# Kernel optimization log

Hardware: AMD Instinct MI355X
Metric: run time of the kernel (lower is better)

Reference implementation:

```python
import jax, jax.numpy as jnp
import numpy as np

A_COEF, B_COEF, C_COEF = 1.0, 0.1, 10.0
KL_COEF = 0.005
EPS = 1e-6

B, P1, F, P2 = 32, 778, 1538, 3000
PARAM_DIM, LATENT = 61, 64


def setup_inputs() -> dict:
    key = jax.random.key(0)
    ks = jax.random.split(key, 9)
    return {
        "recon_x": jax.random.normal(ks[0], (B, PARAM_DIM), jnp.float32),
        "x": jax.random.normal(ks[1], (B, PARAM_DIM), jnp.float32),
        "mu": jax.random.normal(ks[2], (B, LATENT), jnp.float32),
        "logvar": jax.random.normal(ks[3], (B, LATENT), jnp.float32),
        "recon_xyz": jax.random.normal(ks[4], (B, P1, 3), jnp.float32),
        "hand_xyz": jax.random.normal(ks[5], (B, P1, 3), jnp.float32),
        "hand_faces": jax.random.randint(ks[6], (B, F, 3), 0, P1, jnp.int64),
        "obj_pts": jax.random.normal(ks[7], (B, P2, 3), jnp.float32),
        "v_weights": jax.random.uniform(ks[8], (P1,), jnp.float32),
    }


def _verts_normals_single(verts, faces):
    # verts: (V,3), faces: (F,3). PyTorch3D-style area-weighted vertex normals.
    v0 = verts[faces[:, 0]]
    v1 = verts[faces[:, 1]]
    v2 = verts[faces[:, 2]]
    fn = jnp.cross(v1 - v0, v2 - v0)  # (F,3) ~ 2*area*face_normal
    n = (jnp.zeros_like(verts)
         .at[faces[:, 0]].add(fn)
         .at[faces[:, 1]].add(fn)
         .at[faces[:, 2]].add(fn))
    norm = jnp.linalg.norm(n, axis=-1, keepdims=True)
    return n / jnp.maximum(norm, EPS)


_verts_normals = jax.vmap(_verts_normals_single)


def _sqdist(xp, yp):
    # (B,P1,P2) pairwise squared distances
    x2 = jnp.sum(xp * xp, axis=-1)[:, :, None]
    y2 = jnp.sum(yp * yp, axis=-1)[:, None, :]
    return x2 + y2 - 2.0 * jnp.einsum('bpd,bqd->bpq', xp, yp)


def _point2point_signed(xp, yp, x_normals):
    # xp: (B,P1,3) hand, yp: (B,P2,3) object, x_normals: (B,P1,3)
    d2 = _sqdist(xp, yp)
    xidx = jnp.argmin(d2, axis=2)  # (B,P1) nearest object point per hand vert
    yidx = jnp.argmin(d2, axis=1)  # (B,P2) nearest hand vert per object point
    x_near = jnp.take_along_axis(yp, xidx[..., None], axis=1)  # (B,P1,3)
    y_near = jnp.take_along_axis(xp, yidx[..., None], axis=1)  # (B,P2,3)
    x2y = xp - x_near
    y2x = yp - y_near
    y_nn = jnp.take_along_axis(x_normals, yidx[..., None], axis=1)  # (B,P2,3)
    in_out = jnp.sign(jnp.sum(y_nn * y2x, axis=-1))
    y2x_signed = jnp.linalg.norm(y2x, axis=2) * in_out  # (B,P2)
    x2y_signed = jnp.linalg.norm(x2y, axis=2)           # (B,P1)
    return y2x_signed, x2y_signed


def _loss_cnet(verts_rhand, verts_rhand_gt, faces, verts_obj, v_weights):
    v_w2 = jnp.power(v_weights, 1.0 / 2.5)
    rh_n = _verts_normals(verts_rhand, faces)
    rh_n_gt = _verts_normals(verts_rhand_gt, faces)
    o2h, h2o = _point2point_signed(verts_rhand, verts_obj, rh_n)
    o2h_gt, h2o_gt = _point2point_signed(verts_rhand_gt, verts_obj, rh_n_gt)
    w_dist = (o2h_gt < 0.01) & (o2h_gt > -0.005)
    w_neg = o2h < 0.0
    w = jnp.where(w_neg, 1.5, jnp.where(w_dist, 1.0, 0.1))
    loss_h = 35.0 * (1.0 - KL_COEF) * jnp.mean(jnp.abs(jnp.abs(h2o) - jnp.abs(h2o_gt)) * v_w2)
    loss_o = 30.0 * (1.0 - KL_COEF) * jnp.mean(jnp.abs(o2h - o2h_gt) * w)
    return loss_h + loss_o


def reference(recon_x, x, mu, logvar, recon_xyz, hand_xyz, hand_faces, obj_pts, v_weights):
    bsz = recon_x.shape[0]
    param_loss = jnp.sum((recon_x - x) ** 2) / bsz
    recon_loss = jnp.sum((recon_xyz - hand_xyz) ** 2) / hand_xyz.shape[0]
    KLD = -0.5 * jnp.sum(1.0 + logvar - mu ** 2 - jnp.exp(logvar)) / hand_xyz.shape[0]
    cvae_loss = recon_loss + KLD
    ho_loss = _loss_cnet(recon_xyz, hand_xyz, hand_faces, obj_pts, v_weights)
    loss = A_COEF * cvae_loss + B_COEF * param_loss + C_COEF * ho_loss
    return loss, param_loss, ho_loss, recon_loss, KLD
```

## Files before the change

### kernel.cpp

```cpp
#include <hip/hip_runtime.h>
#include <math.h>

#define B 32
#define P1 778
#define NF 1538
#define P2 3000
#define PARAM_DIM 61
#define LATENT 64

#define P1PAD 784
#define NTH 49
#define CHO 192
#define NTO 12
#define NTOH 6
#define NCH 16
#define NPART NCH

#define RED1_BLKS 16
#define HC_BLKS 128
#define OC_BLKS 192
#define QF 385

#define D1_NRM 256
#define D1_TOT (D1_NRM + RED1_BLKS)
#define D2_TOT (NCH * 64)
#define D3_TOT (OC_BLKS + HC_BLKS)

#define NP_OFF  0
#define NP_SZ   (4*2*B*P1*4)
#define OS_OFF  (NP_OFF + NP_SZ)
#define OS_SZ   (2*B*P2)
#define HP_OFF  (OS_OFF + OS_SZ)
#define HP_SZ   (NPART*2*B*P1PAD)
#define R1_OFF  (HP_OFF + HP_SZ)
#define RH_OFF  (R1_OFF + RED1_BLKS*3)
#define RO_OFF  (RH_OFF + HC_BLKS)

typedef __attribute__((ext_vector_type(8))) short bf16x8;
typedef __attribute__((ext_vector_type(4))) float f32x4;
union U4 { uint4 u; bf16x8 v; };

static __device__ __forceinline__ unsigned umin2(unsigned a, unsigned b) { return a < b ? a : b; }
static __device__ __forceinline__ unsigned bhi(float x) { return __float_as_uint(x) >> 16; }
static __device__ __forceinline__ float bres(float x, unsigned h) { return x - __uint_as_float(h << 16); }

template <int CTRL>
static __device__ __forceinline__ float dpp_min(float x) {
  const int xi = __float_as_int(x);
  const int yi = __builtin_amdgcn_update_dpp(xi, xi, CTRL, 0xF, 0xF, false);
  return fminf(x, __int_as_float(yi));
}
static __device__ __forceinline__ float row_min16(float x) {
  x = dpp_min<0xB1>(x);
  x = dpp_min<0x4E>(x);
  x = dpp_min<0x124>(x);
  x = dpp_min<0x128>(x);
  return x;
}

__global__ __launch_bounds__(256) void kd1(
    const float* __restrict__ recon_x, const float* __restrict__ x,
    const float* __restrict__ mu, const float* __restrict__ logvar,
    const float* __restrict__ recon_xyz, const float* __restrict__ hand_xyz,
    const int* __restrict__ faces, float* __restrict__ ws) {
  __shared__ float4 sv[P1];
  __shared__ float sn[4][2336];
  const int tid = threadIdx.x;
  const int bid = blockIdx.x;

  if (bid < D1_NRM) {
    const int q = bid >> 6, r = bid & 63, set = r >> 5, b = r & 31;
    const float* verts = (set == 0 ? recon_xyz : hand_xyz) + b * P1 * 3;
    const int* f = faces + b * NF * 3 + q * QF * 3;
    const int nf = (q < 3) ? QF : (NF - 3 * QF);
    for (int i = tid; i < P1; i += 256)
      sv[i] = make_float4(verts[3*i], verts[3*i+1], verts[3*i+2], 0.f);
    for (int i = tid; i < 4 * 2336; i += 256) ((float*)sn)[i] = 0.f;
    __syncthreads();
    float* s = sn[tid >> 6];
    for (int k = tid; k < nf; k += 256) {
      int i0 = f[3*k], i1 = f[3*k+1], i2 = f[3*k+2];
      float4 v0 = sv[i0], v1 = sv[i1], v2 = sv[i2];
      float e0x = v1.x - v0.x, e0y = v1.y - v0.y, e0z = v1.z - v0.z;
      float e1x = v2.x - v0.x, e1y = v2.y - v0.y, e1z = v2.z - v0.z;
      float fx = e0y * e1z - e0z * e1y;
      float fy = e0z * e1x - e0x * e1z;
      float fz = e0x * e1y - e0y * e1x;
      atomicAdd(&s[3*i0+0], fx); atomicAdd(&s[3*i0+1], fy); atomicAdd(&s[3*i0+2], fz);
      atomicAdd(&s[3*i1+0], fx); atomicAdd(&s[3*i1+1], fy); atomicAdd(&s[3*i1+2], fz);
      atomicAdd(&s[3*i2+0], fx); atomicAdd(&s[3*i2+1], fy); atomicAdd(&s[3*i2+2], fz);
    }
    __syncthreads();
    float4* np = (float4*)(ws + NP_OFF) + (size_t)((q * 2 + set) * B + b) * P1;
    for (int p = tid; p < P1; p += 256) {
      float nx = sn[0][3*p] + sn[1][3*p] + sn[2][3*p] + sn[3][3*p];
      float ny = sn[0][3*p+1] + sn[1][3*p+1] + sn[2][3*p+1] + sn[3][3*p+1];
      float nz = sn[0][3*p+2] + sn[1][3*p+2] + sn[2][3*p+2] + sn[3][3*p+2];
      np[p] = make_float4(nx, ny, nz, 0.f);
    }
  } else {
    const int blk = bid - D1_NRM;
    const int gtid = blk * 256 + tid, stride = RED1_BLKS * 256;
    float sp = 0.f, sr = 0.f, sk = 0.f;
    for (int i = gtid; i < B * PARAM_DIM; i += stride) { float d = recon_x[i] - x[i]; sp += d * d; }
    for (int i = gtid; i < B * P1 * 3; i += stride)    { float d = recon_xyz[i] - hand_xyz[i]; sr += d * d; }
    for (int i = gtid; i < B * LATENT; i += stride)    { float lv = logvar[i], m = mu[i]; sk += 1.f + lv - m * m - expf(lv); }
    for (int off = 32; off > 0; off >>= 1) {
      sp += __shfl_down(sp, off, 64);
      sr += __shfl_down(sr, off, 64);
      sk += __shfl_down(sk, off, 64);
    }
    float* sred = (float*)sn;
    const int wv = tid >> 6;
    if ((tid & 63) == 0) { sred[wv*3] = sp; sred[wv*3+1] = sr; sred[wv*3+2] = sk; }
    __syncthreads();
    if (tid == 0) {
      float a = 0.f, bb = 0.f, c = 0.f;
      for (int w = 0; w < 4; ++w) { a += sred[w*3]; bb += sred[w*3+1]; c += sred[w*3+2]; }
      ws[R1_OFF + blk*3+0] = a; ws[R1_OFF + blk*3+1] = bb; ws[R1_OFF + blk*3+2] = c;
    }
  }
}

__global__ __launch_bounds__(256, 4) void kd2(
    const float* __restrict__ recon_xyz, const float* __restrict__ hand_xyz,
    const float* __restrict__ obj, float* __restrict__ ws) {
  __shared__ float4 sVerts[P1PAD];
  __shared__ float4 sObj[CHO];
  __shared__ unsigned sKeys[4][CHO];

  const int tid = threadIdx.x;
  const int bid = blockIdx.x;
  const int chunk = bid >> 6, rr = bid & 63, set = rr >> 5, b = rr & 31;
  const float* verts = (set == 0 ? recon_xyz : hand_xyz) + b * P1 * 3;
  const float* op = obj + (size_t)b * P2 * 3;

  for (int i = tid; i < P1PAD; i += 256) {
    float vx, vy, vz;
    if (i < P1) { vx = verts[3*i]; vy = verts[3*i+1]; vz = verts[3*i+2]; }
    else        { vx = vy = vz = 1.0e6f; }
    sVerts[i] = make_float4(vx, vy, vz, vx*vx + vy*vy + vz*vz);
  }
  for (int i = tid; i < CHO; i += 256) {
    const int q = chunk * CHO + i;
    float ox, oy, oz;
    if (q < P2) { ox = op[3*q]; oy = op[3*q+1]; oz = op[3*q+2]; }
    else        { ox = oy = oz = 1.0e6f; }
    sObj[i] = make_float4(ox, oy, oz, ox*ox + oy*oy + oz*oz);
  }
  __syncthreads();

  const int l = tid & 63, wv = tid >> 6, g = l >> 4, cl = l & 15;
  U4 bw[NTO];
  #pragma unroll
  for (int j = 0; j < NTO; ++j) {
    const float4 o = sObj[j * 16 + cl];
    unsigned u0 = 0u, u1 = 0u, u2 = 0u, u3 = 0u;
    if (g == 0) {
      const unsigned ohx = bhi(o.x), ohy = bhi(o.y), ohz = bhi(o.z);
      const unsigned olx = bhi(bres(o.x, ohx));
      const unsigned oly = bhi(bres(o.y, ohy));
      u0 = ohx | (ohy << 16);
      u1 = ohz | (ohx << 16);
      u2 = ohy | (ohz << 16);
      u3 = olx | (oly << 16);
    } else if (g == 1) {
      const unsigned ohz = bhi(o.z);
      const unsigned olz = bhi(bres(o.z, ohz));
      const float o2p = o.w + 1.0f;
      const unsigned o2h = bhi(o2p);
      const unsigned o2l = bhi(bres(o2p, o2h));
      u0 = olz | (0x3F80u << 16);
      u1 = 0x3F80u | (o2h << 16);
      u2 = o2l;
      u3 = 0u;
    }
    bw[j].u = make_uint4(u0, u1, u2, u3);
  }

  unsigned om[NTO];
  #pragma unroll
  for (int j = 0; j < NTO; ++j) om[j] = 0xFFFFFFFFu;

  float* hpart = ws + HP_OFF + (size_t)(((chunk * 2) + set) * B + b) * P1PAD;
  const f32x4 czero = {0.f, 0.f, 0.f, 0.f};
  const int nt = (NTH - wv + 3) >> 2;

  for (int s = 0; s < nt; ++s) {
    const int t = wv + 4 * s;
    const int ib = t * 16 + g * 4;
    U4 ac;
    if (l < 32) {
      const float4 v = sVerts[t * 16 + cl];
      if (g == 0) {
        const float sx = -2.f * v.x, sy = -2.f * v.y, sz = -2.f * v.z;
        const unsigned hx = bhi(sx), hy = bhi(sy), hz = bhi(sz);
        const unsigned lx = bhi(bres(sx, hx));
        const unsigned ly = bhi(bres(sy, hy));
        const unsigned lz = bhi(bres(sz, hz));
        ac.u = make_uint4(hx | (hy << 16), hz | (lx << 16),
                          ly | (lz << 16), hx | (hy << 16));
      } else {
        const float sz = -2.f * v.z;
        const unsigned hz = bhi(sz);
        const unsigned h2h = bhi(v.w);
        const unsigned h2l = bhi(bres(v.w, h2h));
        ac.u = make_uint4(hz | (h2h << 16), h2l | (0x3F80u << 16), 0x3F80u, 0u);
      }
    } else {
      ac.u = make_uint4(0u, 0u, 0u, 0u);
    }
    float hm0 = 3.0e38f, hm1 = 3.0e38f, hm2 = 3.0e38f, hm3 = 3.0e38f;
    #pragma unroll
    for (int hs = 0; hs < 2; ++hs) {
      f32x4 dd[NTOH];
      #pragma unroll
      for (int j = 0; j < NTOH; ++j)
        dd[j] = __builtin_amdgcn_mfma_f32_16x16x32_bf16(ac.v, bw[hs * NTOH + j].v, czero, 0, 0, 0);
      #pragma unroll
      for (int j = 0; j < NTOH; ++j) {
        const f32x4 d = dd[j];
        hm0 = fminf(hm0, d[0]); hm1 = fminf(hm1, d[1]);
        hm2 = fminf(hm2, d[2]); hm3 = fminf(hm3, d[3]);
        const unsigned k0 = (__float_as_uint(d[0]) & 0xFFFFFC00u) | (unsigned)(ib + 0);
        const unsigned k1 = (__float_as_uint(d[1]) & 0xFFFFFC00u) | (unsigned)(ib + 1);
        const unsigned k2 = (__float_as_uint(d[2]) & 0xFFFFFC00u) | (unsigned)(ib + 2);
        const unsigned k3 = (__float_as_uint(d[3]) & 0xFFFFFC00u) | (unsigned)(ib + 3);
        om[hs * NTOH + j] = umin2(umin2(umin2(umin2(k0, k1), k2), k3), om[hs * NTOH + j]);
      }
    }
    hm0 = row_min16(hm0);
    hm1 = row_min16(hm1);
    hm2 = row_min16(hm2);
    hm3 = row_min16(hm3);
    if (cl == 0)
      *(float4*)&hpart[ib] = make_float4(hm0 - 1.f, hm1 - 1.f, hm2 - 1.f, hm3 - 1.f);
  }

  #pragma unroll
  for (int j = 0; j < NTO; ++j) {
    unsigned v = umin2(om[j], (unsigned)__shfl_xor((int)om[j], 16, 64));
    v = umin2(v, (unsigned)__shfl_xor((int)v, 32, 64));
    if (l < 16) sKeys[wv][j * 16 + l] = v;
  }
  __syncthreads();

  const float4* npb = (const float4*)(ws + NP_OFF);
  float* os = ws + OS_OFF + (size_t)(set * B + b) * P2;
  for (int i = tid; i < CHO; i += 256) {
    const int q = chunk * CHO + i;
    if (q < P2) {
      const unsigned key = umin2(umin2(sKeys[0][i], sKeys[1][i]),
                                 umin2(sKeys[2][i], sKeys[3][i]));
      int hi = (int)(key & 1023u); if (hi > P1 - 1) hi = P1 - 1;
      const float4 h = sVerts[hi];
      const float4 o = sObj[i];
      const float dx = o.x - h.x, dy = o.y - h.y, dz = o.z - h.z;
      const float d2 = fmaf(dx, dx, fmaf(dy, dy, dz * dz));
      const float4 n0 = npb[(size_t)((0 * 2 + set) * B + b) * P1 + hi];
      const float4 n1 = npb[(size_t)((1 * 2 + set) * B + b) * P1 + hi];
      const float4 n2 = npb[(size_t)((2 * 2 + set) * B + b) * P1 + hi];
      const float4 n3 = npb[(size_t)((3 * 2 + set) * B + b) * P1 + hi];
      const float nx = (n0.x + n1.x) + (n2.x + n3.x);
      const float ny = (n0.y + n1.y) + (n2.y + n3.y);
      const float nz = (n0.z + n1.z) + (n2.z + n3.z);
      const float dt = nx * dx + ny * dy + nz * dz;
      const float sg = (dt > 0.f) ? 1.f : ((dt < 0.f) ? -1.f : 0.f);
      os[q] = sqrtf(d2) * sg;
    }
  }
}

__global__ __launch_bounds__(256) void kd3(const float* __restrict__ vw,
                                           float* __restrict__ ws) {
  __shared__ float sred[4];
  const int tid = threadIdx.x;
  const int bid = blockIdx.x;
  if (bid < OC_BLKS) {
    const int gtid = bid * 256 + tid, stride = OC_BLKS * 256;
    float so = 0.f;
    for (int i = gtid; i < B * P2; i += stride) {
      float osA = ws[OS_OFF + i];
      float osB = ws[OS_OFF + (size_t)B * P2 + i];
      bool wdist = (osB < 0.01f) && (osB > -0.005f);
      float w = (osA < 0.f) ? 1.5f : (wdist ? 1.f : 0.1f);
      so += fabsf(osA - osB) * w;
    }
    for (int off = 32; off > 0; off >>= 1) so += __shfl_down(so, off, 64);
    if ((tid & 63) == 0) sred[tid >> 6] = so;
    __syncthreads();
    if (tid == 0) ws[RO_OFF + bid] = sred[0] + sred[1] + sred[2] + sred[3];
  } else {
    const int blk = bid - OC_BLKS;
    const int gtid = blk * 256 + tid, stride = HC_BLKS * 256;
    float sh = 0.f;
    for (int i = gtid; i < B * P1; i += stride) {
      const int p = i % P1, bb = i / P1;
      const size_t base0 = (size_t)HP_OFF + (size_t)bb * P1PAD + p;
      float m0 = 3.0e38f, m1 = 3.0e38f;
      #pragma unroll
      for (int c = 0; c < NPART; ++c) {
        m0 = fminf(m0, ws[base0 + (size_t)(c*2+0) * B * P1PAD]);
        m1 = fminf(m1, ws[base0 + (size_t)(c*2+1) * B * P1PAD]);
      }
      m0 = fmaxf(m0, 0.f); m1 = fmaxf(m1, 0.f);
      sh += fabsf(sqrtf(m0) - sqrtf(m1)) * powf(vw[p], 0.4f);
    }
    for (int off = 32; off > 0; off >>= 1) sh += __shfl_down(sh, off, 64);
    if ((tid & 63) == 0) sred[tid >> 6] = sh;
    __syncthreads();
    if (tid == 0) ws[RH_OFF + blk] = sred[0] + sred[1] + sred[2] + sred[3];
  }
}

__global__ void kfin(const float* __restrict__ ws, float* __restrict__ out) {
  const int lane = threadIdx.x;
  float sp = 0.f, sr = 0.f, sk = 0.f, sh = 0.f, so = 0.f;
  for (int i = lane; i < RED1_BLKS; i += 64) {
    sp += ws[R1_OFF + i*3+0]; sr += ws[R1_OFF + i*3+1]; sk += ws[R1_OFF + i*3+2];
  }
  for (int i = lane; i < HC_BLKS; i += 64) sh += ws[RH_OFF + i];
  for (int i = lane; i < OC_BLKS; i += 64) so += ws[RO_OFF + i];
  for (int off = 32; off > 0; off >>= 1) {
    sp += __shfl_down(sp, off, 64);
    sr += __shfl_down(sr, off, 64);
    sk += __shfl_down(sk, off, 64);
    sh += __shfl_down(sh, off, 64);
    so += __shfl_down(so, off, 64);
  }
  if (lane == 0) {
    float param_loss = sp / (float)B;
    float recon_loss = sr / (float)B;
    float KLD = -0.5f * sk / (float)B;
    float cvae = recon_loss + KLD;
    float loss_h = 35.f * (1.f - 0.005f) * sh / (float)(B * P1);
    float loss_o = 30.f * (1.f - 0.005f) * so / (float)(B * P2);
    float ho = loss_h + loss_o;
    out[0] = cvae + 0.1f * param_loss + 10.f * ho;
    out[1] = param_loss;
    out[2] = ho;
    out[3] = recon_loss;
    out[4] = KLD;
  }
}

extern "C" void kernel_launch(void* const* d_in, const int* in_sizes, int n_in,
                              void* d_out, int out_size, void* d_ws, size_t ws_size,
                              hipStream_t stream) {
  const float* recon_x   = (const float*)d_in[0];
  const float* x         = (const float*)d_in[1];
  const float* mu        = (const float*)d_in[2];
  const float* logvar    = (const float*)d_in[3];
  const float* recon_xyz = (const float*)d_in[4];
  const float* hand_xyz  = (const float*)d_in[5];
  const int*   faces     = (const int*)d_in[6];
  const float* obj       = (const float*)d_in[7];
  const float* vw        = (const float*)d_in[8];
  float* ws = (float*)d_ws;
  float* out = (float*)d_out;

  kd1<<<dim3(D1_TOT), 256, 0, stream>>>(recon_x, x, mu, logvar,
                                        recon_xyz, hand_xyz, faces, ws);
  kd2<<<dim3(D2_TOT), 256, 0, stream>>>(recon_xyz, hand_xyz, obj, ws);
  kd3<<<dim3(D3_TOT), 256, 0, stream>>>(vw, ws);
  kfin<<<1, 64, 0, stream>>>(ws, out);
}
```

Before: 115.5 us.

## Partition vertex normals by vertex range and fold final reduction into kd3

The normal computation now splits work by vertex range (200 vertices per block) instead of by face range. Each block scans all faces and only accumulates into its own vertices, so a single normal buffer is written and kd2 loads one float4 per lookup instead of four partials. The separate kfin launch is removed: kd3 uses an atomic counter with threadfences so the last block does the final reduction. The cost is redundant face processing in kd1, in exchange for one fewer kernel launch and fewer global reads in kd2.

New measurement: 138.2 us. 1.2x slower.

```diff
diff --git a/kernel.cpp b/kernel.cpp
--- a/kernel.cpp
+++ b/kernel.cpp
@@ -19,7 +19,7 @@
 #define RED1_BLKS 16
 #define HC_BLKS 128
 #define OC_BLKS 192
-#define QF 385
+#define VR 200
 
 #define D1_NRM 256
 #define D1_TOT (D1_NRM + RED1_BLKS)
@@ -27,7 +27,7 @@
 #define D3_TOT (OC_BLKS + HC_BLKS)
 
 #define NP_OFF  0
-#define NP_SZ   (4*2*B*P1*4)
+#define NP_SZ   (2*B*P1*4)
 #define OS_OFF  (NP_OFF + NP_SZ)
 #define OS_SZ   (2*B*P2)
 #define HP_OFF  (OS_OFF + OS_SZ)
@@ -35,6 +35,7 @@
 #define R1_OFF  (HP_OFF + HP_SZ)
 #define RH_OFF  (R1_OFF + RED1_BLKS*3)
 #define RO_OFF  (RH_OFF + HC_BLKS)
+#define CNT_OFF (RO_OFF + OC_BLKS)
 
 typedef __attribute__((ext_vector_type(8))) short bf16x8;
 typedef __attribute__((ext_vector_type(4))) float f32x4;
@@ -64,21 +65,22 @@
     const float* __restrict__ recon_xyz, const float* __restrict__ hand_xyz,
     const int* __restrict__ faces, float* __restrict__ ws) {
   __shared__ float4 sv[P1];
-  __shared__ float sn[4][2336];
+  __shared__ float sn[4][3 * VR];
   const int tid = threadIdx.x;
   const int bid = blockIdx.x;
 
   if (bid < D1_NRM) {
     const int q = bid >> 6, r = bid & 63, set = r >> 5, b = r & 31;
+    const int lo = q * VR;
+    const int hi = (lo + VR < P1) ? lo + VR : P1;
     const float* verts = (set == 0 ? recon_xyz : hand_xyz) + b * P1 * 3;
-    const int* f = faces + b * NF * 3 + q * QF * 3;
-    const int nf = (q < 3) ? QF : (NF - 3 * QF);
+    const int* f = faces + b * NF * 3;
     for (int i = tid; i < P1; i += 256)
       sv[i] = make_float4(verts[3*i], verts[3*i+1], verts[3*i+2], 0.f);
-    for (int i = tid; i < 4 * 2336; i += 256) ((float*)sn)[i] = 0.f;
+    for (int i = tid; i < 4 * 3 * VR; i += 256) ((float*)sn)[i] = 0.f;
     __syncthreads();
     float* s = sn[tid >> 6];
-    for (int k = tid; k < nf; k += 256) {
+    for (int k = tid; k < NF; k += 256) {
       int i0 = f[3*k], i1 = f[3*k+1], i2 = f[3*k+2];
       float4 v0 = sv[i0], v1 = sv[i1], v2 = sv[i2];
       float e0x = v1.x - v0.x, e0y = v1.y - v0.y, e0z = v1.z - v0.z;
@@ -86,20 +88,31 @@
       float fx = e0y * e1z - e0z * e1y;
       float fy = e0z * e1x - e0x * e1z;
       float fz = e0x * e1y - e0y * e1x;
-      atomicAdd(&s[3*i0+0], fx); atomicAdd(&s[3*i0+1], fy); atomicAdd(&s[3*i0+2], fz);
-      atomicAdd(&s[3*i1+0], fx); atomicAdd(&s[3*i1+1], fy); atomicAdd(&s[3*i1+2], fz);
-      atomicAdd(&s[3*i2+0], fx); atomicAdd(&s[3*i2+1], fy); atomicAdd(&s[3*i2+2], fz);
-    }
-    __syncthreads();
-    float4* np = (float4*)(ws + NP_OFF) + (size_t)((q * 2 + set) * B + b) * P1;
-    for (int p = tid; p < P1; p += 256) {
-      float nx = sn[0][3*p] + sn[1][3*p] + sn[2][3*p] + sn[3][3*p];
-      float ny = sn[0][3*p+1] + sn[1][3*p+1] + sn[2][3*p+1] + sn[3][3*p+1];
-      float nz = sn[0][3*p+2] + sn[1][3*p+2] + sn[2][3*p+2] + sn[3][3*p+2];
+      if (i0 >= lo && i0 < hi) {
+        int j = (i0 - lo) * 3;
+        atomicAdd(&s[j+0], fx); atomicAdd(&s[j+1], fy); atomicAdd(&s[j+2], fz);
+      }
+      if (i1 >= lo && i1 < hi) {
+        int j = (i1 - lo) * 3;
+        atomicAdd(&s[j+0], fx); atomicAdd(&s[j+1], fy); atomicAdd(&s[j+2], fz);
+      }
+      if (i2 >= lo && i2 < hi) {
+        int j = (i2 - lo) * 3;
+        atomicAdd(&s[j+0], fx); atomicAdd(&s[j+1], fy); atomicAdd(&s[j+2], fz);
+      }
+    }
+    __syncthreads();
+    float4* np = (float4*)(ws + NP_OFF) + (size_t)(set * B + b) * P1;
+    for (int p = lo + tid; p < hi; p += 256) {
+      const int j = (p - lo) * 3;
+      float nx = sn[0][j]   + sn[1][j]   + sn[2][j]   + sn[3][j];
+      float ny = sn[0][j+1] + sn[1][j+1] + sn[2][j+1] + sn[3][j+1];
+      float nz = sn[0][j+2] + sn[1][j+2] + sn[2][j+2] + sn[3][j+2];
       np[p] = make_float4(nx, ny, nz, 0.f);
     }
   } else {
     const int blk = bid - D1_NRM;
+    if (blk == 0 && tid == 0) ws[CNT_OFF] = 0.f;
     const int gtid = blk * 256 + tid, stride = RED1_BLKS * 256;
     float sp = 0.f, sr = 0.f, sk = 0.f;
     for (int i = gtid; i < B * PARAM_DIM; i += stride) { float d = recon_x[i] - x[i]; sp += d * d; }
@@ -245,7 +258,7 @@
   }
   __syncthreads();
 
-  const float4* npb = (const float4*)(ws + NP_OFF);
+  const float4* np = (const float4*)(ws + NP_OFF) + (size_t)(set * B + b) * P1;
   float* os = ws + OS_OFF + (size_t)(set * B + b) * P2;
   for (int i = tid; i < CHO; i += 256) {
     const int q = chunk * CHO + i;
@@ -257,14 +270,8 @@
       const float4 o = sObj[i];
       const float dx = o.x - h.x, dy = o.y - h.y, dz = o.z - h.z;
       const float d2 = fmaf(dx, dx, fmaf(dy, dy, dz * dz));
-      const float4 n0 = npb[(size_t)((0 * 2 + set) * B + b) * P1 + hi];
-      const float4 n1 = npb[(size_t)((1 * 2 + set) * B + b) * P1 + hi];
-      const float4 n2 = npb[(size_t)((2 * 2 + set) * B + b) * P1 + hi];
-      const float4 n3 = npb[(size_t)((3 * 2 + set) * B + b) * P1 + hi];
-      const float nx = (n0.x + n1.x) + (n2.x + n3.x);
-      const float ny = (n0.y + n1.y) + (n2.y + n3.y);
-      const float nz = (n0.z + n1.z) + (n2.z + n3.z);
-      const float dt = nx * dx + ny * dy + nz * dz;
+      const float4 n = np[hi];
+      const float dt = n.x * dx + n.y * dy + n.z * dz;
       const float sg = (dt > 0.f) ? 1.f : ((dt < 0.f) ? -1.f : 0.f);
       os[q] = sqrtf(d2) * sg;
     }
@@ -272,8 +279,10 @@
 }
 
 __global__ __launch_bounds__(256) void kd3(const float* __restrict__ vw,
-                                           float* __restrict__ ws) {
+                                           float* __restrict__ ws,
+                                           float* __restrict__ out) {
   __shared__ float sred[4];
+  __shared__ int lastFlag;
   const int tid = threadIdx.x;
   const int bid = blockIdx.x;
   if (bid < OC_BLKS) {
@@ -311,36 +320,45 @@
     __syncthreads();
     if (tid == 0) ws[RH_OFF + blk] = sred[0] + sred[1] + sred[2] + sred[3];
   }
-}
-
-__global__ void kfin(const float* __restrict__ ws, float* __restrict__ out) {
-  const int lane = threadIdx.x;
-  float sp = 0.f, sr = 0.f, sk = 0.f, sh = 0.f, so = 0.f;
-  for (int i = lane; i < RED1_BLKS; i += 64) {
-    sp += ws[R1_OFF + i*3+0]; sr += ws[R1_OFF + i*3+1]; sk += ws[R1_OFF + i*3+2];
-  }
-  for (int i = lane; i < HC_BLKS; i += 64) sh += ws[RH_OFF + i];
-  for (int i = lane; i < OC_BLKS; i += 64) so += ws[RO_OFF + i];
-  for (int off = 32; off > 0; off >>= 1) {
-    sp += __shfl_down(sp, off, 64);
-    sr += __shfl_down(sr, off, 64);
-    sk += __shfl_down(sk, off, 64);
-    sh += __shfl_down(sh, off, 64);
-    so += __shfl_down(so, off, 64);
-  }
-  if (lane == 0) {
-    float param_loss = sp / (float)B;
-    float recon_loss = sr / (float)B;
-    float KLD = -0.5f * sk / (float)B;
-    float cvae = recon_loss + KLD;
-    float loss_h = 35.f * (1.f - 0.005f) * sh / (float)(B * P1);
-    float loss_o = 30.f * (1.f - 0.005f) * so / (float)(B * P2);
-    float ho = loss_h + loss_o;
-    out[0] = cvae + 0.1f * param_loss + 10.f * ho;
-    out[1] = param_loss;
-    out[2] = ho;
-    out[3] = recon_loss;
-    out[4] = KLD;
+
+  __threadfence();
+  if (tid == 0) {
+    const int t = atomicAdd((int*)(ws + CNT_OFF), 1);
+    lastFlag = (t == D3_TOT - 1);
+  }
+  __syncthreads();
+  if (lastFlag) {
+    __threadfence();
+    if (tid < 64) {
+      const int lane = tid;
+      float sp = 0.f, sr = 0.f, sk = 0.f, sh = 0.f, so = 0.f;
+      for (int i = lane; i < RED1_BLKS; i += 64) {
+        sp += ws[R1_OFF + i*3+0]; sr += ws[R1_OFF + i*3+1]; sk += ws[R1_OFF + i*3+2];
+      }
+      for (int i = lane; i < HC_BLKS; i += 64) sh += ws[RH_OFF + i];
+      for (int i = lane; i < OC_BLKS; i += 64) so += ws[RO_OFF + i];
+      for (int off = 32; off > 0; off >>= 1) {
+        sp += __shfl_down(sp, off, 64);
+        sr += __shfl_down(sr, off, 64);
+        sk += __shfl_down(sk, off, 64);
+        sh += __shfl_down(sh, off, 64);
+        so += __shfl_down(so, off, 64);
+      }
+      if (lane == 0) {
+        float param_loss = sp / (float)B;
+        float recon_loss = sr / (float)B;
+        float KLD = -0.5f * sk / (float)B;
+        float cvae = recon_loss + KLD;
+        float loss_h = 35.f * (1.f - 0.005f) * sh / (float)(B * P1);
+        float loss_o = 30.f * (1.f - 0.005f) * so / (float)(B * P2);
+        float ho = loss_h + loss_o;
+        out[0] = cvae + 0.1f * param_loss + 10.f * ho;
+        out[1] = param_loss;
+        out[2] = ho;
+        out[3] = recon_loss;
+        out[4] = KLD;
+      }
+    }
   }
 }
 
@@ -362,6 +380,5 @@
   kd1<<<dim3(D1_TOT), 256, 0, stream>>>(recon_x, x, mu, logvar,
                                         recon_xyz, hand_xyz, faces, ws);
   kd2<<<dim3(D2_TOT), 256, 0, stream>>>(recon_xyz, hand_xyz, obj, ws);
-  kd3<<<dim3(D3_TOT), 256, 0, stream>>>(vw, ws);
-  kfin<<<1, 64, 0, stream>>>(ws, out);
-}
+  kd3<<<dim3(D3_TOT), 256, 0, stream>>>(vw, ws, out);
+}
```

## Merge normals and nearest-neighbour kernels, move signing to reduce, fold final sum

Applied to the files above, without the earlier changes.

Fuses the vertex-normal, small-reduction and distance/argmin kernels into one launch with a shared-memory union. This is possible because the signed-distance step that needs the normals now runs in the reduction kernel, which reads the stored argmin keys and recomputes distances and signs. The separate final kernel is replaced by a last-block-done atomic counter, cutting the launch chain from four kernels to two. In exchange the reduce kernel does scattered gathers of vertices and normals, and the normal accumulation uses two shared copies instead of four, so more threads contend on each shared atomic.

Measured after the change: 146.9 us. 27.1% more time.

```diff
diff --git a/kernel.cpp b/kernel.cpp
--- a/kernel.cpp
+++ b/kernel.cpp
@@ -21,9 +21,9 @@
 #define OC_BLKS 192
 #define QF 385
 
-#define D1_NRM 256
-#define D1_TOT (D1_NRM + RED1_BLKS)
-#define D2_TOT (NCH * 64)
+#define M_D2  (NCH * 64)
+#define M_NRM 256
+#define M_TOT (M_D2 + M_NRM + RED1_BLKS)
 #define D3_TOT (OC_BLKS + HC_BLKS)
 
 #define NP_OFF  0
@@ -35,6 +35,7 @@
 #define R1_OFF  (HP_OFF + HP_SZ)
 #define RH_OFF  (R1_OFF + RED1_BLKS*3)
 #define RO_OFF  (RH_OFF + HC_BLKS)
+#define CNT_OFF (RO_OFF + OC_BLKS)
 
 typedef __attribute__((ext_vector_type(8))) short bf16x8;
 typedef __attribute__((ext_vector_type(4))) float f32x4;
@@ -58,29 +59,158 @@
   return x;
 }
 
-__global__ __launch_bounds__(256) void kd1(
+union SMem {
+  struct { float4 sv[P1]; float sn[2][2336]; } d1;
+  struct { float4 sVerts[P1PAD]; float4 sObj[CHO]; unsigned sKeys[4][CHO]; } d2;
+};
+
+__global__ __launch_bounds__(256, 4) void kd12(
     const float* __restrict__ recon_x, const float* __restrict__ x,
     const float* __restrict__ mu, const float* __restrict__ logvar,
     const float* __restrict__ recon_xyz, const float* __restrict__ hand_xyz,
-    const int* __restrict__ faces, float* __restrict__ ws) {
-  __shared__ float4 sv[P1];
-  __shared__ float sn[4][2336];
+    const int* __restrict__ faces, const float* __restrict__ obj,
+    float* __restrict__ ws) {
+  __shared__ SMem sm;
   const int tid = threadIdx.x;
   const int bid = blockIdx.x;
 
-  if (bid < D1_NRM) {
-    const int q = bid >> 6, r = bid & 63, set = r >> 5, b = r & 31;
+  if (bid < M_D2) {
+    const int chunk = bid >> 6, rr = bid & 63, set = rr >> 5, b = rr & 31;
+    const float* verts = (set == 0 ? recon_xyz : hand_xyz) + b * P1 * 3;
+    const float* op = obj + (size_t)b * P2 * 3;
+
+    for (int i = tid; i < P1PAD; i += 256) {
+      float vx, vy, vz;
+      if (i < P1) { vx = verts[3*i]; vy = verts[3*i+1]; vz = verts[3*i+2]; }
+      else        { vx = vy = vz = 1.0e6f; }
+      sm.d2.sVerts[i] = make_float4(vx, vy, vz, vx*vx + vy*vy + vz*vz);
+    }
+    for (int i = tid; i < CHO; i += 256) {
+      const int q = chunk * CHO + i;
+      float ox, oy, oz;
+      if (q < P2) { ox = op[3*q]; oy = op[3*q+1]; oz = op[3*q+2]; }
+      else        { ox = oy = oz = 1.0e6f; }
+      sm.d2.sObj[i] = make_float4(ox, oy, oz, ox*ox + oy*oy + oz*oz);
+    }
+    __syncthreads();
+
+    const int l = tid & 63, wv = tid >> 6, g = l >> 4, cl = l & 15;
+    U4 bw[NTO];
+    #pragma unroll
+    for (int j = 0; j < NTO; ++j) {
+      const float4 o = sm.d2.sObj[j * 16 + cl];
+      unsigned u0 = 0u, u1 = 0u, u2 = 0u, u3 = 0u;
+      if (g == 0) {
+        const unsigned ohx = bhi(o.x), ohy = bhi(o.y), ohz = bhi(o.z);
+        const unsigned olx = bhi(bres(o.x, ohx));
+        const unsigned oly = bhi(bres(o.y, ohy));
+        u0 = ohx | (ohy << 16);
+        u1 = ohz | (ohx << 16);
+        u2 = ohy | (ohz << 16);
+        u3 = olx | (oly << 16);
+      } else if (g == 1) {
+        const unsigned ohz = bhi(o.z);
+        const unsigned olz = bhi(bres(o.z, ohz));
+        const float o2p = o.w + 1.0f;
+        const unsigned o2h = bhi(o2p);
+        const unsigned o2l = bhi(bres(o2p, o2h));
+        u0 = olz | (0x3F80u << 16);
+        u1 = 0x3F80u | (o2h << 16);
+        u2 = o2l;
+        u3 = 0u;
+      }
+      bw[j].u = make_uint4(u0, u1, u2, u3);
+    }
+
+    unsigned om[NTO];
+    #pragma unroll
+    for (int j = 0; j < NTO; ++j) om[j] = 0xFFFFFFFFu;
+
+    float* hpart = ws + HP_OFF + (size_t)(((chunk * 2) + set) * B + b) * P1PAD;
+    const f32x4 czero = {0.f, 0.f, 0.f, 0.f};
+    const int nt = (NTH - wv + 3) >> 2;
+
+    for (int s = 0; s < nt; ++s) {
+      const int t = wv + 4 * s;
+      const int ib = t * 16 + g * 4;
+      U4 ac;
+      if (l < 32) {
+        const float4 v = sm.d2.sVerts[t * 16 + cl];
+        if (g == 0) {
+          const float sx = -2.f * v.x, sy = -2.f * v.y, sz = -2.f * v.z;
+          const unsigned hx = bhi(sx), hy = bhi(sy), hz = bhi(sz);
+          const unsigned lx = bhi(bres(sx, hx));
+          const unsigned ly = bhi(bres(sy, hy));
+          const unsigned lz = bhi(bres(sz, hz));
+          ac.u = make_uint4(hx | (hy << 16), hz | (lx << 16),
+                            ly | (lz << 16), hx | (hy << 16));
+        } else {
+          const float sz = -2.f * v.z;
+          const unsigned hz = bhi(sz);
+          const unsigned h2h = bhi(v.w);
+          const unsigned h2l = bhi(bres(v.w, h2h));
+          ac.u = make_uint4(hz | (h2h << 16), h2l | (0x3F80u << 16), 0x3F80u, 0u);
+        }
+      } else {
+        ac.u = make_uint4(0u, 0u, 0u, 0u);
+      }
+      float hm0 = 3.0e38f, hm1 = 3.0e38f, hm2 = 3.0e38f, hm3 = 3.0e38f;
+      #pragma unroll
+      for (int hs = 0; hs < 2; ++hs) {
+        f32x4 dd[NTOH];
+        #pragma unroll
+        for (int j = 0; j < NTOH; ++j)
+          dd[j] = __builtin_amdgcn_mfma_f32_16x16x32_bf16(ac.v, bw[hs * NTOH + j].v, czero, 0, 0, 0);
+        #pragma unroll
+        for (int j = 0; j < NTOH; ++j) {
+          const f32x4 d = dd[j];
+          hm0 = fminf(hm0, d[0]); hm1 = fminf(hm1, d[1]);
+          hm2 = fminf(hm2, d[2]); hm3 = fminf(hm3, d[3]);
+          const unsigned k0 = (__float_as_uint(d[0]) & 0xFFFFFC00u) | (unsigned)(ib + 0);
+          const unsigned k1 = (__float_as_uint(d[1]) & 0xFFFFFC00u) | (unsigned)(ib + 1);
+          const unsigned k2 = (__float_as_uint(d[2]) & 0xFFFFFC00u) | (unsigned)(ib + 2);
+          const unsigned k3 = (__float_as_uint(d[3]) & 0xFFFFFC00u) | (unsigned)(ib + 3);
+          om[hs * NTOH + j] = umin2(umin2(umin2(umin2(k0, k1), k2), k3), om[hs * NTOH + j]);
+        }
+      }
+      hm0 = row_min16(hm0);
+      hm1 = row_min16(hm1);
+      hm2 = row_min16(hm2);
+      hm3 = row_min16(hm3);
+      if (cl == 0)
+        *(float4*)&hpart[ib] = make_float4(hm0 - 1.f, hm1 - 1.f, hm2 - 1.f, hm3 - 1.f);
+    }
+
+    #pragma unroll
+    for (int j = 0; j < NTO; ++j) {
+      unsigned v = umin2(om[j], (unsigned)__shfl_xor((int)om[j], 16, 64));
+      v = umin2(v, (unsigned)__shfl_xor((int)v, 32, 64));
+      if (l < 16) sm.d2.sKeys[wv][j * 16 + l] = v;
+    }
+    __syncthreads();
+
+    unsigned* os = (unsigned*)(ws + OS_OFF) + (size_t)(set * B + b) * P2;
+    for (int i = tid; i < CHO; i += 256) {
+      const int q = chunk * CHO + i;
+      if (q < P2)
+        os[q] = umin2(umin2(sm.d2.sKeys[0][i], sm.d2.sKeys[1][i]),
+                      umin2(sm.d2.sKeys[2][i], sm.d2.sKeys[3][i]));
+    }
+
+  } else if (bid < M_D2 + M_NRM) {
+    const int t = bid - M_D2;
+    const int q = t >> 6, r = t & 63, set = r >> 5, b = r & 31;
     const float* verts = (set == 0 ? recon_xyz : hand_xyz) + b * P1 * 3;
     const int* f = faces + b * NF * 3 + q * QF * 3;
     const int nf = (q < 3) ? QF : (NF - 3 * QF);
     for (int i = tid; i < P1; i += 256)
-      sv[i] = make_float4(verts[3*i], verts[3*i+1], verts[3*i+2], 0.f);
-    for (int i = tid; i < 4 * 2336; i += 256) ((float*)sn)[i] = 0.f;
-    __syncthreads();
-    float* s = sn[tid >> 6];
+      sm.d1.sv[i] = make_float4(verts[3*i], verts[3*i+1], verts[3*i+2], 0.f);
+    for (int i = tid; i < 2 * 2336; i += 256) ((float*)sm.d1.sn)[i] = 0.f;
+    __syncthreads();
+    float* s = sm.d1.sn[tid >> 7];
     for (int k = tid; k < nf; k += 256) {
       int i0 = f[3*k], i1 = f[3*k+1], i2 = f[3*k+2];
-      float4 v0 = sv[i0], v1 = sv[i1], v2 = sv[i2];
+      float4 v0 = sm.d1.sv[i0], v1 = sm.d1.sv[i1], v2 = sm.d1.sv[i2];
       float e0x = v1.x - v0.x, e0y = v1.y - v0.y, e0z = v1.z - v0.z;
       float e1x = v2.x - v0.x, e1y = v2.y - v0.y, e1z = v2.z - v0.z;
       float fx = e0y * e1z - e0z * e1y;
@@ -93,13 +223,14 @@
     __syncthreads();
     float4* np = (float4*)(ws + NP_OFF) + (size_t)((q * 2 + set) * B + b) * P1;
     for (int p = tid; p < P1; p += 256) {
-      float nx = sn[0][3*p] + sn[1][3*p] + sn[2][3*p] + sn[3][3*p];
-      float ny = sn[0][3*p+1] + sn[1][3*p+1] + sn[2][3*p+1] + sn[3][3*p+1];
-      float nz = sn[0][3*p+2] + sn[1][3*p+2] + sn[2][3*p+2] + sn[3][3*p+2];
+      float nx = sm.d1.sn[0][3*p]   + sm.d1.sn[1][3*p];
+      float ny = sm.d1.sn[0][3*p+1] + sm.d1.sn[1][3*p+1];
+      float nz = sm.d1.sn[0][3*p+2] + sm.d1.sn[1][3*p+2];
       np[p] = make_float4(nx, ny, nz, 0.f);
     }
   } else {
-    const int blk = bid - D1_NRM;
+    const int blk = bid - M_D2 - M_NRM;
+    if (blk == 0 && tid == 0) ((int*)(ws + CNT_OFF))[0] = 0;
     const int gtid = blk * 256 + tid, stride = RED1_BLKS * 256;
     float sp = 0.f, sr = 0.f, sk = 0.f;
     for (int i = gtid; i < B * PARAM_DIM; i += stride) { float d = recon_x[i] - x[i]; sp += d * d; }
@@ -110,7 +241,7 @@
       sr += __shfl_down(sr, off, 64);
       sk += __shfl_down(sk, off, 64);
     }
-    float* sred = (float*)sn;
+    float* sred = (float*)sm.d1.sn;
     const int wv = tid >> 6;
     if ((tid & 63) == 0) { sred[wv*3] = sp; sred[wv*3+1] = sr; sred[wv*3+2] = sk; }
     __syncthreads();
@@ -122,166 +253,46 @@
   }
 }
 
-__global__ __launch_bounds__(256, 4) void kd2(
+__global__ __launch_bounds__(256) void kd3(
+    const float* __restrict__ vw,
     const float* __restrict__ recon_xyz, const float* __restrict__ hand_xyz,
-    const float* __restrict__ obj, float* __restrict__ ws) {
-  __shared__ float4 sVerts[P1PAD];
-  __shared__ float4 sObj[CHO];
-  __shared__ unsigned sKeys[4][CHO];
-
-  const int tid = threadIdx.x;
-  const int bid = blockIdx.x;
-  const int chunk = bid >> 6, rr = bid & 63, set = rr >> 5, b = rr & 31;
-  const float* verts = (set == 0 ? recon_xyz : hand_xyz) + b * P1 * 3;
-  const float* op = obj + (size_t)b * P2 * 3;
-
-  for (int i = tid; i < P1PAD; i += 256) {
-    float vx, vy, vz;
-    if (i < P1) { vx = verts[3*i]; vy = verts[3*i+1]; vz = verts[3*i+2]; }
-    else        { vx = vy = vz = 1.0e6f; }
-    sVerts[i] = make_float4(vx, vy, vz, vx*vx + vy*vy + vz*vz);
-  }
-  for (int i = tid; i < CHO; i += 256) {
-    const int q = chunk * CHO + i;
-    float ox, oy, oz;
-    if (q < P2) { ox = op[3*q]; oy = op[3*q+1]; oz = op[3*q+2]; }
-    else        { ox = oy = oz = 1.0e6f; }
-    sObj[i] = make_float4(ox, oy, oz, ox*ox + oy*oy + oz*oz);
-  }
-  __syncthreads();
-
-  const int l = tid & 63, wv = tid >> 6, g = l >> 4, cl = l & 15;
-  U4 bw[NTO];
-  #pragma unroll
-  for (int j = 0; j < NTO; ++j) {
-    const float4 o = sObj[j * 16 + cl];
-    unsigned u0 = 0u, u1 = 0u, u2 = 0u, u3 = 0u;
-    if (g == 0) {
-      const unsigned ohx = bhi(o.x), ohy = bhi(o.y), ohz = bhi(o.z);
-      const unsigned olx = bhi(bres(o.x, ohx));
-      const unsigned oly = bhi(bres(o.y, ohy));
-      u0 = ohx | (ohy << 16);
-      u1 = ohz | (ohx << 16);
-      u2 = ohy | (ohz << 16);
-      u3 = olx | (oly << 16);
-    } else if (g == 1) {
-      const unsigned ohz = bhi(o.z);
-      const unsigned olz = bhi(bres(o.z, ohz));
-      const float o2p = o.w + 1.0f;
-      const unsigned o2h = bhi(o2p);
-      const unsigned o2l = bhi(bres(o2p, o2h));
-      u0 = olz | (0x3F80u << 16);
-      u1 = 0x3F80u | (o2h << 16);
-      u2 = o2l;
-      u3 = 0u;
-    }
-    bw[j].u = make_uint4(u0, u1, u2, u3);
-  }
-
-  unsigned om[NTO];
-  #pragma unroll
-  for (int j = 0; j < NTO; ++j) om[j] = 0xFFFFFFFFu;
-
-  float* hpart = ws + HP_OFF + (size_t)(((chunk * 2) + set) * B + b) * P1PAD;
-  const f32x4 czero = {0.f, 0.f, 0.f, 0.f};
-  const int nt = (NTH - wv + 3) >> 2;
-
-  for (int s = 0; s < nt; ++s) {
-    const int t = wv + 4 * s;
-    const int ib = t * 16 + g * 4;
-    U4 ac;
-    if (l < 32) {
-      const float4 v = sVerts[t * 16 + cl];
-      if (g == 0) {
-        const float sx = -2.f * v.x, sy = -2.f * v.y, sz = -2.f * v.z;
-        const unsigned hx = bhi(sx), hy = bhi(sy), hz = bhi(sz);
-        const unsigned lx = bhi(bres(sx, hx));
-        const unsigned ly = bhi(bres(sy, hy));
-        const unsigned lz = bhi(bres(sz, hz));
-        ac.u = make_uint4(hx | (hy << 16), hz | (lx << 16),
-                          ly | (lz << 16), hx | (hy << 16));
-      } else {
-        const float sz = -2.f * v.z;
-        const unsigned hz = bhi(sz);
-        const unsigned h2h = bhi(v.w);
-        const unsigned h2l = bhi(bres(v.w, h2h));
-        ac.u = make_uint4(hz | (h2h << 16), h2l | (0x3F80u << 16), 0x3F80u, 0u);
-      }
-    } else {
-      ac.u = make_uint4(0u, 0u, 0u, 0u);
-    }
-    float hm0 = 3.0e38f, hm1 = 3.0e38f, hm2 = 3.0e38f, hm3 = 3.0e38f;
-    #pragma unroll
-    for (int hs = 0; hs < 2; ++hs) {
-      f32x4 dd[NTOH];
-      #pragma unroll
-      for (int j = 0; j < NTOH; ++j)
-        dd[j] = __builtin_amdgcn_mfma_f32_16x16x32_bf16(ac.v, bw[hs * NTOH + j].v, czero, 0, 0, 0);
-      #pragma unroll
-      for (int j = 0; j < NTOH; ++j) {
-        const f32x4 d = dd[j];
-        hm0 = fminf(hm0, d[0]); hm1 = fminf(hm1, d[1]);
-        hm2 = fminf(hm2, d[2]); hm3 = fminf(hm3, d[3]);
-        const unsigned k0 = (__float_as_uint(d[0]) & 0xFFFFFC00u) | (unsigned)(ib + 0);
-        const unsigned k1 = (__float_as_uint(d[1]) & 0xFFFFFC00u) | (unsigned)(ib + 1);
-        const unsigned k2 = (__float_as_uint(d[2]) & 0xFFFFFC00u) | (unsigned)(ib + 2);
-        const unsigned k3 = (__float_as_uint(d[3]) & 0xFFFFFC00u) | (unsigned)(ib + 3);
-        om[hs * NTOH + j] = umin2(umin2(umin2(umin2(k0, k1), k2), k3), om[hs * NTOH + j]);
-      }
-    }
-    hm0 = row_min16(hm0);
-    hm1 = row_min16(hm1);
-    hm2 = row_min16(hm2);
-    hm3 = row_min16(hm3);
-    if (cl == 0)
-      *(float4*)&hpart[ib] = make_float4(hm0 - 1.f, hm1 - 1.f, hm2 - 1.f, hm3 - 1.f);
-  }
-
-  #pragma unroll
-  for (int j = 0; j < NTO; ++j) {
-    unsigned v = umin2(om[j], (unsigned)__shfl_xor((int)om[j], 16, 64));
-    v = umin2(v, (unsigned)__shfl_xor((int)v, 32, 64));
-    if (l < 16) sKeys[wv][j * 16 + l] = v;
-  }
-  __syncthreads();
-
-  const float4* npb = (const float4*)(ws + NP_OFF);
-  float* os = ws + OS_OFF + (size_t)(set * B + b) * P2;
-  for (int i = tid; i < CHO; i += 256) {
-    const int q = chunk * CHO + i;
-    if (q < P2) {
-      const unsigned key = umin2(umin2(sKeys[0][i], sKeys[1][i]),
-                                 umin2(sKeys[2][i], sKeys[3][i]));
-      int hi = (int)(key & 1023u); if (hi > P1 - 1) hi = P1 - 1;
-      const float4 h = sVerts[hi];
-      const float4 o = sObj[i];
-      const float dx = o.x - h.x, dy = o.y - h.y, dz = o.z - h.z;
-      const float d2 = fmaf(dx, dx, fmaf(dy, dy, dz * dz));
-      const float4 n0 = npb[(size_t)((0 * 2 + set) * B + b) * P1 + hi];
-      const float4 n1 = npb[(size_t)((1 * 2 + set) * B + b) * P1 + hi];
-      const float4 n2 = npb[(size_t)((2 * 2 + set) * B + b) * P1 + hi];
-      const float4 n3 = npb[(size_t)((3 * 2 + set) * B + b) * P1 + hi];
-      const float nx = (n0.x + n1.x) + (n2.x + n3.x);
-      const float ny = (n0.y + n1.y) + (n2.y + n3.y);
-      const float nz = (n0.z + n1.z) + (n2.z + n3.z);
-      const float dt = nx * dx + ny * dy + nz * dz;
-      const float sg = (dt > 0.f) ? 1.f : ((dt < 0.f) ? -1.f : 0.f);
-      os[q] = sqrtf(d2) * sg;
-    }
-  }
-}
-
-__global__ __launch_bounds__(256) void kd3(const float* __restrict__ vw,
-                                           float* __restrict__ ws) {
+    const float* __restrict__ obj,
+    float* __restrict__ ws, float* __restrict__ out) {
   __shared__ float sred[4];
+  __shared__ int lastFlag;
   const int tid = threadIdx.x;
   const int bid = blockIdx.x;
   if (bid < OC_BLKS) {
+    const unsigned* osu = (const unsigned*)(ws + OS_OFF);
+    const float4* npb = (const float4*)(ws + NP_OFF);
     const int gtid = bid * 256 + tid, stride = OC_BLKS * 256;
     float so = 0.f;
     for (int i = gtid; i < B * P2; i += stride) {
-      float osA = ws[OS_OFF + i];
-      float osB = ws[OS_OFF + (size_t)B * P2 + i];
+      const int b = i / P2, q = i - b * P2;
+      int hiA = (int)(osu[i] & 1023u);                  if (hiA > P1-1) hiA = P1-1;
+      int hiB = (int)(osu[(size_t)B * P2 + i] & 1023u); if (hiB > P1-1) hiB = P1-1;
+      const float* op = obj + ((size_t)b * P2 + q) * 3;
+      const float ox = op[0], oy = op[1], oz = op[2];
+      const float* va = recon_xyz + ((size_t)b * P1 + hiA) * 3;
+      const float* vb = hand_xyz  + ((size_t)b * P1 + hiB) * 3;
+      const float dxA = ox - va[0], dyA = oy - va[1], dzA = oz - va[2];
+      const float dxB = ox - vb[0], dyB = oy - vb[1], dzB = oz - vb[2];
+      const float d2A = fmaf(dxA, dxA, fmaf(dyA, dyA, dzA * dzA));
+      const float d2B = fmaf(dxB, dxB, fmaf(dyB, dyB, dzB * dzB));
+      float nAx = 0.f, nAy = 0.f, nAz = 0.f, nBx = 0.f, nBy = 0.f, nBz = 0.f;
+      #pragma unroll
+      for (int qt = 0; qt < 4; ++qt) {
+        const float4 na = npb[(size_t)((qt * 2 + 0) * B + b) * P1 + hiA];
+        const float4 nb = npb[(size_t)((qt * 2 + 1) * B + b) * P1 + hiB];
+        nAx += na.x; nAy += na.y; nAz += na.z;
+        nBx += nb.x; nBy += nb.y; nBz += nb.z;
+      }
+      const float dtA = nAx * dxA + nAy * dyA + nAz * dzA;
+      const float dtB = nBx * dxB + nBy * dyB + nBz * dzB;
+      const float sgA = (dtA > 0.f) ? 1.f : ((dtA < 0.f) ? -1.f : 0.f);
+      const float sgB = (dtB > 0.f) ? 1.f : ((dtB < 0.f) ? -1.f : 0.f);
+      const float osA = sqrtf(d2A) * sgA;
+      const float osB = sqrtf(d2B) * sgB;
       bool wdist = (osB < 0.01f) && (osB > -0.005f);
       float w = (osA < 0.f) ? 1.5f : (wdist ? 1.f : 0.1f);
       so += fabsf(osA - osB) * w;
@@ -311,36 +322,45 @@
     __syncthreads();
     if (tid == 0) ws[RH_OFF + blk] = sred[0] + sred[1] + sred[2] + sred[3];
   }
-}
-
-__global__ void kfin(const float* __restrict__ ws, float* __restrict__ out) {
-  const int lane = threadIdx.x;
-  float sp = 0.f, sr = 0.f, sk = 0.f, sh = 0.f, so = 0.f;
-  for (int i = lane; i < RED1_BLKS; i += 64) {
-    sp += ws[R1_OFF + i*3+0]; sr += ws[R1_OFF + i*3+1]; sk += ws[R1_OFF + i*3+2];
+
+  __threadfence();
+  if (tid == 0) {
+    const int t = atomicAdd((int*)(ws + CNT_OFF), 1);
+    lastFlag = (t == D3_TOT - 1);
   }
-  for (int i = lane; i < HC_BLKS; i += 64) sh += ws[RH_OFF + i];
-  for (int i = lane; i < OC_BLKS; i += 64) so += ws[RO_OFF + i];
-  for (int off = 32; off > 0; off >>= 1) {
-    sp += __shfl_down(sp, off, 64);
-    sr += __shfl_down(sr, off, 64);
-    sk += __shfl_down(sk, off, 64);
-    sh += __shfl_down(sh, off, 64);
-    so += __shfl_down(so, off, 64);
-  }
-  if (lane == 0) {
-    float param_loss = sp / (float)B;
-    float recon_loss = sr / (float)B;
-    float KLD = -0.5f * sk / (float)B;
-    float cvae = recon_loss + KLD;
-    float loss_h = 35.f * (1.f - 0.005f) * sh / (float)(B * P1);
-    float loss_o = 30.f * (1.f - 0.005f) * so / (float)(B * P2);
-    float ho = loss_h + loss_o;
-    out[0] = cvae + 0.1f * param_loss + 10.f * ho;
-    out[1] = param_loss;
-    out[2] = ho;
-    out[3] = recon_loss;
-    out[4] = KLD;
+  __syncthreads();
+  if (lastFlag) {
+    __threadfence();
+    if (tid < 64) {
+      const int lane = tid;
+      float sp = 0.f, sr = 0.f, sk = 0.f, sh = 0.f, so = 0.f;
+      for (int i = lane; i < RED1_BLKS; i += 64) {
+        sp += ws[R1_OFF + i*3+0]; sr += ws[R1_OFF + i*3+1]; sk += ws[R1_OFF + i*3+2];
+      }
+      for (int i = lane; i < HC_BLKS; i += 64) sh += ws[RH_OFF + i];
+      for (int i = lane; i < OC_BLKS; i += 64) so += ws[RO_OFF + i];
+      for (int off = 32; off > 0; off >>= 1) {
+        sp += __shfl_down(sp, off, 64);
+        sr += __shfl_down(sr, off, 64);
+        sk += __shfl_down(sk, off, 64);
+        sh += __shfl_down(sh, off, 64);
+        so += __shfl_down(so, off, 64);
+      }
+      if (lane == 0) {
+        float param_loss = sp / (float)B;
+        float recon_loss = sr / (float)B;
+        float KLD = -0.5f * sk / (float)B;
+        float cvae = recon_loss + KLD;
+        float loss_h = 35.f * (1.f - 0.005f) * sh / (float)(B * P1);
+        float loss_o = 30.f * (1.f - 0.005f) * so / (float)(B * P2);
+        float ho = loss_h + loss_o;
+        out[0] = cvae + 0.1f * param_loss + 10.f * ho;
+        out[1] = param_loss;
+        out[2] = ho;
+        out[3] = recon_loss;
+        out[4] = KLD;
+      }
+    }
   }
 }
 
@@ -359,9 +379,7 @@
   float* ws = (float*)d_ws;
   float* out = (float*)d_out;
 
-  kd1<<<dim3(D1_TOT), 256, 0, stream>>>(recon_x, x, mu, logvar,
-                                        recon_xyz, hand_xyz, faces, ws);
-  kd2<<<dim3(D2_TOT), 256, 0, stream>>>(recon_xyz, hand_xyz, obj, ws);
-  kd3<<<dim3(D3_TOT), 256, 0, stream>>>(vw, ws);
-  kfin<<<1, 64, 0, stream>>>(ws, out);
-}
+  kd12<<<dim3(M_TOT), 256, 0, stream>>>(recon_x, x, mu, logvar,
+                                        recon_xyz, hand_xyz, faces, obj, ws);
+  kd3<<<dim3(D3_TOT), 256, 0, stream>>>(vw, recon_xyz, hand_xyz, obj, ws, out);
+}
```
